# Kernel tuning notes

Hardware: AMD Instinct MI355X
Metric: run time of the kernel (lower is better)

The kernel has to match this reference:

```python
import jax, jax.numpy as jnp
import numpy as np

B, C, H, W = 2, 96, 40, 40
DIN, N, R, K = 192, 16, 6, 4  # d_inner, d_state, dt_rank, k_group


def silu(x):
    return x * jax.nn.sigmoid(x)


def dwconv3x3(x, w, b):
    # depthwise 3x3, SAME padding; w: (DIN,1,3,3)
    y = jax.lax.conv_general_dilated(x, w, (1, 1), [(1, 1), (1, 1)],
                                     feature_group_count=x.shape[1])
    return y + b[None, :, None, None]


def cross_scan(x):
    # (B,C,H,W) -> (B,4,C,L): row-major, col-major, and their reverses
    b, c, h, w = x.shape
    x0 = x.reshape(b, c, h * w)
    x1 = x.transpose(0, 1, 3, 2).reshape(b, c, h * w)
    return jnp.stack([x0, x1, x0[..., ::-1], x1[..., ::-1]], axis=1)


def cross_merge(y, h, w):
    # (B,4,C,H,W) -> (B,C,L)
    b, k, c = y.shape[0], y.shape[1], y.shape[2]
    y = y.reshape(b, k, c, h * w)
    y = y[:, :2] + y[:, 2:][..., ::-1]
    y1 = y[:, 1].reshape(b, c, w, h).transpose(0, 1, 3, 2).reshape(b, c, h * w)
    return y[:, 0] + y1


def selective_scan(u, dt, A, Bm, Cm, Dv, dbias):
    # u, dt: (B,K,DIN,L); A: (K*DIN,N); Bm, Cm: (B,K,N,L); Dv: (K*DIN,); dbias: (K*DIN,)
    b, k, d, l = u.shape
    n = A.shape[1]
    A4 = A.reshape(k, d, n)
    dt = jax.nn.softplus(dt + dbias.reshape(1, k, d, 1))
    # discretize: dA = exp(dt*A), dBu = dt*B*u  -> shapes (B,K,D,L,N)
    dA = jnp.exp(dt[..., None] * A4[None, :, :, None, :])
    dBu = dt[..., None] * Bm.transpose(0, 1, 3, 2)[:, :, None, :, :] * u[..., None]

    def combine(c1, c2):
        a1, b1 = c1
        a2, b2 = c2
        return a1 * a2, a2 * b1 + b2

    _, h = jax.lax.associative_scan(combine, (dA, dBu), axis=3)  # h: (B,K,D,L,N)
    y = jnp.einsum('bkdln,bknl->bkdl', h, Cm)
    return y + Dv.reshape(1, k, d, 1) * u


def ln2d(x, g, b):
    # LayerNorm over channel dim (channel_first LayerNorm2d)
    mu = x.mean(axis=1, keepdims=True)
    var = jnp.mean((x - mu) ** 2, axis=1, keepdims=True)
    xn = (x - mu) / jnp.sqrt(var + 1e-5)
    return xn * g[None, :, None, None] + b[None, :, None, None]


def setup_inputs():
    key = jax.random.key(0)
    ks = jax.random.split(key, 24)

    def rn(k, shape, s=0.02):
        return jax.random.normal(k, shape, dtype=jnp.float32) * s

    A_log = jnp.tile(jnp.log(jnp.arange(1, N + 1, dtype=jnp.float32))[None, :], (K * DIN, 1))
    return {
        'x_rgb': jax.random.normal(ks[0], (B, C, H, W), jnp.float32),
        'x_e': jax.random.normal(ks[1], (B, C, H, W), jnp.float32),
        'in_proj_w': rn(ks[2], (DIN, C)),
        'in_proj_mx_w': rn(ks[3], (DIN, C)),
        'conv_w': rn(ks[4], (DIN, 1, 3, 3), 0.1),
        'conv_b': jnp.zeros((DIN,), jnp.float32),
        'xproj1_w': rn(ks[5], (K, R + 2 * N, DIN)),
        'xproj2_w': rn(ks[6], (K, R + 2 * N, DIN)),
        'dtproj1_w': rn(ks[7], (K, DIN, R), 0.1),
        'dtproj1_b': rn(ks[8], (K, DIN), 0.1) - 4.0,
        'dtproj2_w': rn(ks[9], (K, DIN, R), 0.1),
        'dtproj2_b': rn(ks[10], (K, DIN), 0.1) - 4.0,
        'A_log_1': A_log,
        'A_log_2': A_log,
        'D_1': jnp.ones((K * DIN,), jnp.float32),
        'D_2': jnp.ones((K * DIN,), jnp.float32),
        'norm1_g': jnp.ones((DIN,), jnp.float32),
        'norm1_b': jnp.zeros((DIN,), jnp.float32),
        'norm2_g': jnp.ones((DIN,), jnp.float32),
        'norm2_b': jnp.zeros((DIN,), jnp.float32),
        'fc1_w1': rn(ks[11], (DIN // 16, DIN), 0.05),
        'fc1_w2': rn(ks[12], (DIN, DIN // 16), 0.05),
        'fc2_w1': rn(ks[13], (DIN // 16, DIN), 0.05),
        'fc2_w2': rn(ks[14], (DIN, DIN // 16), 0.05),
        'out_proj_w': rn(ks[15], (C, 2 * DIN)),
    }


def reference(x_rgb, x_e, in_proj_w, in_proj_mx_w, conv_w, conv_b, xproj1_w, xproj2_w,
              dtproj1_w, dtproj1_b, dtproj2_w, dtproj2_b, A_log_1, A_log_2, D_1, D_2,
              norm1_g, norm1_b, norm2_g, norm2_b, fc1_w1, fc1_w2, fc2_w1, fc2_w2, out_proj_w):
    # in_proj (1x1 conv style Linear2d)
    xr = jnp.einsum('oc,bchw->bohw', in_proj_w, x_rgb)
    xe = jnp.einsum('oc,bchw->bohw', in_proj_mx_w, x_e)
    # shared depthwise conv + SiLU
    xr = silu(dwconv3x3(xr, conv_w, conv_b))
    xe = silu(dwconv3x3(xe, conv_w, conv_b))
    b, d, h, w = xr.shape

    xs_r = cross_scan(xr)  # (B,K,DIN,L)
    xs_e = cross_scan(xe)

    def proj(xs, xp_w, dt_w):
        t = jnp.einsum('bkdl,kcd->bkcl', xs, xp_w)  # grouped 1x1 conv1d
        dts, Bm, Cm = jnp.split(t, [R, R + N], axis=2)
        dts = jnp.einsum('bkrl,kdr->bkdl', dts, dt_w)
        return dts, Bm, Cm

    d_r, B_r, C_r = proj(xs_r, xproj1_w, dtproj1_w)
    d_e, B_e, C_e = proj(xs_e, xproj2_w, dtproj2_w)

    # cross attention: rgb scan consumes C and D of the other modality
    y_r = selective_scan(xs_r, d_r, -jnp.exp(A_log_1), B_r, C_e, D_2, dtproj1_b.reshape(-1))
    y_e = selective_scan(xs_e, d_e, -jnp.exp(A_log_2), B_e, C_r, D_1, dtproj2_b.reshape(-1))

    y_r = cross_merge(y_r.reshape(b, K, d, h, w), h, w).reshape(b, d, h, w)
    y_e = cross_merge(y_e.reshape(b, K, d, h, w), h, w).reshape(b, d, h, w)
    y_r = ln2d(y_r, norm1_g, norm1_b)
    y_e = ln2d(y_e, norm2_g, norm2_b)

    # cross squeeze-excitation
    sq_r = xr.mean(axis=(2, 3))
    sq_e = xe.mean(axis=(2, 3))
    exc_r = jax.nn.sigmoid(silu(sq_r @ fc1_w1.T) @ fc1_w2.T)
    exc_e = jax.nn.sigmoid(silu(sq_e @ fc2_w1.T) @ fc2_w2.T)
    y_r = y_r * exc_e[:, :, None, None]
    y_e = y_e * exc_r[:, :, None, None]

    y = jnp.concatenate([y_r, y_e], axis=1)  # (B, 2*DIN, H, W)
    return jnp.einsum('oc,bchw->bohw', out_proj_w, y)
```

## Files before the change

kernel.cpp:

```cpp
#include <hip/hip_runtime.h>
#include <math.h>

#define BN   2
#define CIN  96
#define HH   40
#define WW   40
#define LL   1600
#define DIN  192
#define NS   16
#define RR   6
#define KK   4
#define CH   25

__device__ __forceinline__ float sigmoidf_(float x){ return 1.0f/(1.0f+expf(-x)); }
__device__ __forceinline__ float softplus_fast(float x){
  return x > 20.0f ? x : __logf(1.0f + __expf(x));
}

__device__ __forceinline__ void pow_tree(float R, float* p){
  float R2 = R * R;
  float R4 = R2 * R2;
  float R8 = R4 * R4;
  p[0]  = R;        p[1]  = R2;       p[2]  = R2 * R;   p[3]  = R4;
  p[4]  = R4 * R;   p[5]  = R4 * R2;  p[6]  = R4 * p[2];p[7]  = R8;
  p[8]  = R8 * R;   p[9]  = R8 * R2;  p[10] = R8 * p[2];p[11] = R8 * R4;
  p[12] = R8 * p[4];p[13] = R8 * p[5];p[14] = R8 * p[6];p[15] = R8 * R8;
}

__global__ void k_inproj(const float* __restrict__ x_rgb, const float* __restrict__ x_e,
                         const float* __restrict__ w_rgb, const float* __restrict__ w_e,
                         float* __restrict__ xproj){
  __shared__ float xin[16][100];
  int l0 = blockIdx.x * 16;
  int mb = blockIdx.y;
  int m = mb / BN, b = mb % BN;
  const float* xsrc = (m == 0 ? x_rgb : x_e) + (size_t)b * CIN * LL;
  const float* w    = (m == 0 ? w_rgb : w_e);
  for (int idx = threadIdx.x; idx < CIN * 16; idx += 256){
    int c = idx >> 4, px = idx & 15;
    xin[px][c] = xsrc[c * LL + l0 + px];
  }
  __syncthreads();
  int px = threadIdx.x & 15;
  int o0 = (threadIdx.x >> 4) * 12;
  float acc[12];
  #pragma unroll
  for (int i = 0; i < 12; ++i) acc[i] = 0.f;
  const float4* xv = reinterpret_cast<const float4*>(xin[px]);
  for (int cc = 0; cc < CIN / 4; ++cc){
    float4 x4 = xv[cc];
    #pragma unroll
    for (int i = 0; i < 12; ++i){
      float4 w4 = *reinterpret_cast<const float4*>(w + (o0 + i) * CIN + cc * 4);
      acc[i] += w4.x * x4.x + w4.y * x4.y + w4.z * x4.z + w4.w * x4.w;
    }
  }
  #pragma unroll
  for (int i = 0; i < 12; ++i)
    xproj[((size_t)mb * DIN + o0 + i) * LL + l0 + px] = acc[i];
}

__global__ void k_conv(const float* __restrict__ xproj, const float* __restrict__ conv_w,
                       const float* __restrict__ conv_b, float* __restrict__ x_act,
                       float* __restrict__ x_actT, float* __restrict__ u_chA,
                       float* __restrict__ u_chT, float* __restrict__ sq){
  __shared__ float pl[LL];
  __shared__ float sact[LL + HH];
  __shared__ float red[4];
  int d  = blockIdx.x;
  int mb = blockIdx.y;
  const float* src = xproj + ((size_t)mb * DIN + d) * LL;
  for (int p = threadIdx.x; p < LL; p += blockDim.x) pl[p] = src[p];
  __syncthreads();
  float cw[9];
  #pragma unroll
  for (int j = 0; j < 9; ++j) cw[j] = conv_w[d * 9 + j];
  float bias = conv_b[d];
  float* dst = x_act + ((size_t)mb * DIN + d) * LL;
  float lsum = 0.f;
  for (int p = threadIdx.x; p < LL; p += blockDim.x){
    int py = p / WW, px = p % WW;
    float acc = bias;
    #pragma unroll
    for (int dy = -1; dy <= 1; ++dy){
      int yy = py + dy;
      if (yy < 0 || yy >= HH) continue;
      #pragma unroll
      for (int dx = -1; dx <= 1; ++dx){
        int xx = px + dx;
        if (xx < 0 || xx >= WW) continue;
        acc += cw[(dy + 1) * 3 + (dx + 1)] * pl[yy * WW + xx];
      }
    }
    float s = acc * sigmoidf_(acc);
    dst[p] = s;
    sact[p + p / WW] = s;
    lsum += s;
  }
  #pragma unroll
  for (int off = 32; off; off >>= 1) lsum += __shfl_down(lsum, off);
  if ((threadIdx.x & 63) == 0) red[threadIdx.x >> 6] = lsum;
  __syncthreads();
  if (threadIdx.x == 0)
    sq[mb * DIN + d] = (red[0] + red[1] + red[2] + red[3]) * (1.0f / LL);
  size_t po = ((size_t)mb * DIN + d) * LL;
  float* dstT = x_actT + po;
  float* uA   = u_chA + po;
  float* uT   = u_chT + po;
  for (int q = threadIdx.x; q < LL; q += blockDim.x){
    int lt = (q % WW) * WW + q / WW;
    dstT[q] = sact[lt + lt / WW];
    int l = (q & 63) * CH + (q >> 6);
    uA[q] = sact[l + l / WW];
    int pt = (l % WW) * WW + l / WW;
    uT[q] = sact[pt + pt / WW];
  }
}

__global__ void k_xproj(const float* __restrict__ x_act, const float* __restrict__ x_actT,
                        const float* __restrict__ xp1, const float* __restrict__ xp2,
                        float* __restrict__ tdt_ch, float* __restrict__ B_ch,
                        float* __restrict__ C_ch){
  int l0 = blockIdx.x * 64;
  int k  = blockIdx.y;
  int mb = blockIdx.z; int m = mb / BN;
  const float* xw = (m == 0 ? xp1 : xp2) + k * 38 * DIN;
  const float* xa = ((k & 1) ? x_actT : x_act) + (size_t)mb * DIN * LL;
  bool rev = (k >= 2);
  int ll = threadIdx.x & 63;
  int g  = threadIdx.x >> 6;
  int c0 = g * 10;
  int l  = l0 + ll; if (rev) l = LL - 1 - l;
  const float* xcol = xa + l;
  float acc[10];
  #pragma unroll
  for (int i = 0; i < 10; ++i) acc[i] = 0.f;
  if (g < 3){
    for (int dd = 0; dd < DIN; ++dd){
      float xv = xcol[(size_t)dd * LL];
      #pragma unroll
      for (int i = 0; i < 10; ++i) acc[i] += xw[(c0 + i) * DIN + dd] * xv;
    }
  } else {
    for (int dd = 0; dd < DIN; ++dd){
      float xv = xcol[(size_t)dd * LL];
      #pragma unroll
      for (int i = 0; i < 8; ++i) acc[i] += xw[(c0 + i) * DIN + dd] * xv;
    }
  }
  int mbk = mb * KK + k;
  int lq = l0 + ll;
  int q = (lq % CH) * 64 + lq / CH;
  int nc = (g < 3) ? 10 : 8;
  for (int i = 0; i < nc; ++i){
    int c = c0 + i;
    float v = acc[i];
    if (c < RR){
      tdt_ch[((size_t)mbk * RR + c) * LL + q] = v;
    } else if (c < RR + NS){
      int n = c - RR;
      B_ch[(((size_t)mbk * 4 + (n >> 2)) * LL + q) * 4 + (n & 3)] = v;
    } else {
      int n = c - RR - NS;
      C_ch[(((size_t)mbk * 4 + (n >> 2)) * LL + q) * 4 + (n & 3)] = v;
    }
  }
}

__global__ void __launch_bounds__(256, 3) k_scan(
    const float* __restrict__ u_chA, const float* __restrict__ u_chT,
    const float* __restrict__ tdt_all, const float* __restrict__ B_ch,
    const float* __restrict__ C_ch,
    const float* __restrict__ Alog1, const float* __restrict__ Alog2,
    const float* __restrict__ D1, const float* __restrict__ D2,
    const float* __restrict__ dtw1, const float* __restrict__ dtb1,
    const float* __restrict__ dtw2, const float* __restrict__ dtb2,
    float* __restrict__ y_px){
  __shared__ float ystage[4][LL];
  __shared__ float dt_lds[4][LL];
  int wv   = threadIdx.x >> 6;
  int lane = threadIdx.x & 63;
  int chain = blockIdx.x * 4 + wv;
  int d   = chain % DIN;
  int mbk = chain / DIN;
  int k   = mbk % KK;
  int mb  = mbk / KK;
  int m = mb / BN, b = mb % BN;
  int kd = k * DIN + d;
  bool rev = (k >= 2);

  const float* Alog = (m == 0 ? Alog1 : Alog2) + kd * NS;
  float An[NS];
  bool fastA = true;
  #pragma unroll
  for (int n = 0; n < NS; ++n){
    An[n] = -__expf(Alog[n]);
    fastA = fastA && (fabsf(An[n] + (float)(n + 1)) <= 1e-4f * (float)(n + 1));
  }
  float Dv = (m == 0 ? D2 : D1)[kd];
  const float* dtw = (m == 0 ? dtw1 : dtw2) + kd * RR;
  float w0 = dtw[0], w1 = dtw[1], w2 = dtw[2], w3 = dtw[3], w4 = dtw[4], w5 = dtw[5];
  float dbias = (m == 0 ? dtb1 : dtb2)[kd];

  const float* t0 = tdt_all + (size_t)mbk * RR * LL;
  for (int s = 0; s < CH; ++s){
    int q = s * 64 + lane;
    float dtpre = w0 * t0[q] + w1 * t0[LL + q] + w2 * t0[2 * LL + q]
                + w3 * t0[3 * LL + q] + w4 * t0[4 * LL + q] + w5 * t0[5 * LL + q] + dbias;
    dt_lds[wv][q] = softplus_fast(dtpre);
  }

  const float4* B0 = reinterpret_cast<const float4*>(B_ch) + (size_t)mbk * 4 * LL;
  int mbk_o = ((1 - m) * BN + b) * KK + k;
  const float4* C0 = reinterpret_cast<const float4*>(C_ch) + (size_t)mbk_o * 4 * LL;
  const float* urow = ((k & 1) ? u_chT : u_chA) + ((size_t)mb * DIN + d) * LL;

  float h[NS];
  #pragma unroll
  for (int n = 0; n < NS; ++n) h[n] = 0.f;
  float Sdt = 0.f;

  if (fastA){
    #pragma unroll 5
    for (int s = 0; s < CH; ++s){
      int q = s * 64 + lane;
      float dt = dt_lds[wv][q];
      Sdt += dt;
      float u  = urow[rev ? (LL - 1 - q) : q];
      float du = dt * u;
      float4 b0 = B0[q], b1 = B0[LL + q], b2 = B0[2 * LL + q], b3 = B0[3 * LL + q];
      float4 c0 = C0[q], c1 = C0[LL + q], c2 = C0[2 * LL + q], c3 = C0[3 * LL + q];
      float Bv[NS] = {b0.x,b0.y,b0.z,b0.w, b1.x,b1.y,b1.z,b1.w,
                      b2.x,b2.y,b2.z,b2.w, b3.x,b3.y,b3.z,b3.w};
      float Cv[NS] = {c0.x,c0.y,c0.z,c0.w, c1.x,c1.y,c1.z,c1.w,
                      c2.x,c2.y,c2.z,c2.w, c3.x,c3.y,c3.z,c3.w};
      float p[NS];
      pow_tree(__expf(-dt), p);
      float y0 = Dv * u, y1 = 0.f, y2 = 0.f, y3 = 0.f;
      #pragma unroll
      for (int n = 0; n < NS; ++n){
        h[n] = p[n] * h[n] + du * Bv[n];
        float t = h[n] * Cv[n];
        if      ((n & 3) == 0) y0 += t;
        else if ((n & 3) == 1) y1 += t;
        else if ((n & 3) == 2) y2 += t;
        else                   y3 += t;
      }
      ystage[wv][lane * CH + s] = (y0 + y1) + (y2 + y3);
    }
  } else {
    #pragma unroll 5
    for (int s = 0; s < CH; ++s){
      int q = s * 64 + lane;
      float dt = dt_lds[wv][q];
      Sdt += dt;
      float u  = urow[rev ? (LL - 1 - q) : q];
      float du = dt * u;
      float4 b0 = B0[q], b1 = B0[LL + q], b2 = B0[2 * LL + q], b3 = B0[3 * LL + q];
      float4 c0 = C0[q], c1 = C0[LL + q], c2 = C0[2 * LL + q], c3 = C0[3 * LL + q];
      float Bv[NS] = {b0.x,b0.y,b0.z,b0.w, b1.x,b1.y,b1.z,b1.w,
                      b2.x,b2.y,b2.z,b2.w, b3.x,b3.y,b3.z,b3.w};
      float Cv[NS] = {c0.x,c0.y,c0.z,c0.w, c1.x,c1.y,c1.z,c1.w,
                      c2.x,c2.y,c2.z,c2.w, c3.x,c3.y,c3.z,c3.w};
      float y0 = Dv * u, y1 = 0.f, y2 = 0.f, y3 = 0.f;
      #pragma unroll
      for (int n = 0; n < NS; ++n){
        float dA = __expf(dt * An[n]);
        h[n] = dA * h[n] + du * Bv[n];
        float t = h[n] * Cv[n];
        if      ((n & 3) == 0) y0 += t;
        else if ((n & 3) == 1) y1 += t;
        else if ((n & 3) == 2) y2 += t;
        else                   y3 += t;
      }
      ystage[wv][lane * CH + s] = (y0 + y1) + (y2 + y3);
    }
  }
  float aP[NS];
  if (fastA){
    pow_tree(__expf(-Sdt), aP);
  } else {
    #pragma unroll
    for (int n = 0; n < NS; ++n) aP[n] = __expf(Sdt * An[n]);
  }

  #pragma unroll
  for (int off = 1; off < 64; off <<= 1){
    #pragma unroll
    for (int n = 0; n < NS; ++n){
      float ap = __shfl_up(aP[n], off);
      float bp = __shfl_up(h[n],  off);
      if (lane >= off){
        h[n]  = aP[n] * bp + h[n];
        aP[n] = aP[n] * ap;
      }
    }
  }
  #pragma unroll
  for (int n = 0; n < NS; ++n){
    float v = __shfl_up(h[n], 1);
    h[n] = (lane == 0) ? 0.f : v;
  }

  if (fastA){
    float cum = 0.f;
    #pragma unroll 5
    for (int s = 0; s < CH; ++s){
      int q = s * 64 + lane;
      cum += dt_lds[wv][q];
      float Rc = __expf(-cum);
      float4 c0 = C0[q], c1 = C0[LL + q], c2 = C0[2 * LL + q], c3 = C0[3 * LL + q];
      float Cv[NS] = {c0.x,c0.y,c0.z,c0.w, c1.x,c1.y,c1.z,c1.w,
                      c2.x,c2.y,c2.z,c2.w, c3.x,c3.y,c3.z,c3.w};
      float p[NS];
      pow_tree(Rc, p);
      float s0 = 0.f, s1 = 0.f, s2 = 0.f, s3 = 0.f;
      #pragma unroll
      for (int n = 0; n < NS; ++n){
        float t = h[n] * p[n] * Cv[n];
        if      ((n & 3) == 0) s0 += t;
        else if ((n & 3) == 1) s1 += t;
        else if ((n & 3) == 2) s2 += t;
        else                   s3 += t;
      }
      ystage[wv][lane * CH + s] += (s0 + s1) + (s2 + s3);
    }
  } else {
    float cum = 0.f;
    #pragma unroll 5
    for (int s = 0; s < CH; ++s){
      int q = s * 64 + lane;
      cum += dt_lds[wv][q];
      float4 c0 = C0[q], c1 = C0[LL + q], c2 = C0[2 * LL + q], c3 = C0[3 * LL + q];
      float Cv[NS] = {c0.x,c0.y,c0.z,c0.w, c1.x,c1.y,c1.z,c1.w,
                      c2.x,c2.y,c2.z,c2.w, c3.x,c3.y,c3.z,c3.w};
      float s0 = 0.f, s1 = 0.f, s2 = 0.f, s3 = 0.f;
      #pragma unroll
      for (int n = 0; n < NS; ++n){
        float t = h[n] * __expf(cum * An[n]) * Cv[n];
        if      ((n & 3) == 0) s0 += t;
        else if ((n & 3) == 1) s1 += t;
        else if ((n & 3) == 2) s2 += t;
        else                   s3 += t;
      }
      ystage[wv][lane * CH + s] += (s0 + s1) + (s2 + s3);
    }
  }

  float* yo = y_px + (size_t)chain * LL;
  for (int qq = lane; qq < LL; qq += 64){
    int l;
    if      (k == 0) l = qq;
    else if (k == 1) l = (qq % WW) * WW + qq / WW;
    else if (k == 2) l = LL - 1 - qq;
    else             { int qt = (qq % WW) * WW + qq / WW; l = LL - 1 - qt; }
    yo[qq] = ystage[wv][l];
  }
}

__global__ void __launch_bounds__(256) k_mergeout(
    const float* __restrict__ y_px, const float* __restrict__ sq,
    const float* __restrict__ fc1_w1, const float* __restrict__ fc1_w2,
    const float* __restrict__ fc2_w1, const float* __restrict__ fc2_w2,
    const float* __restrict__ n1g, const float* __restrict__ n1b,
    const float* __restrict__ n2g, const float* __restrict__ n2b,
    const float* __restrict__ wout, float* __restrict__ out){
  __shared__ float acc[2 * DIN][9];
  __shared__ float yt[8][388];
  __shared__ float ps[2][8][16], ps2[2][8][16];
  __shared__ float mu_s[2][8], inv_s[2][8];
  __shared__ float sqs[2][DIN];
  __shared__ float hid[2][12];
  __shared__ float exc_s[2][DIN];
  int p0 = blockIdx.x * 8;
  int b  = blockIdx.y;
  int tid = threadIdx.x;
  for (int idx = tid; idx < 2 * DIN * 8; idx += 256){
    int pp = idx & 7, row = idx >> 3;
    int mm = (row >= DIN), dd = row - mm * DIN;
    const float* yb = y_px + ((size_t)(mm * BN + b) * KK * DIN + dd) * LL + p0 + pp;
    acc[row][pp] = yb[0] + yb[(size_t)DIN * LL]
                 + yb[2 * (size_t)DIN * LL] + yb[3 * (size_t)DIN * LL];
  }
  for (int i = tid; i < 2 * DIN; i += 256){
    int mm = (i >= DIN), dd = i - mm * DIN;
    sqs[mm][dd] = sq[((1 - mm) * BN + b) * DIN + dd];
  }
  __syncthreads();
  if (tid < 24){
    int mm = tid / 12, j = tid - mm * 12;
    const float* w1 = (mm == 1 ? fc1_w1 : fc2_w1);
    float a = 0.f;
    for (int cch = 0; cch < DIN; ++cch) a += w1[j * DIN + cch] * sqs[mm][cch];
    hid[mm][j] = a * sigmoidf_(a);
  }
  {
    int pp = tid & 7, mm = (tid >> 3) & 1, g = tid >> 4;
    float s = 0.f, s2 = 0.f;
    #pragma unroll 4
    for (int j = 0; j < 12; ++j){
      float v = acc[mm * DIN + g * 12 + j][pp];
      s += v; s2 += v * v;
    }
    ps[mm][pp][g] = s; ps2[mm][pp][g] = s2;
  }
  __syncthreads();
  if (tid < 16){
    int mm = tid >> 3, pp = tid & 7;
    float s = 0.f, s2 = 0.f;
    #pragma unroll
    for (int g = 0; g < 16; ++g){ s += ps[mm][pp][g]; s2 += ps2[mm][pp][g]; }
    float mu  = s * (1.0f / DIN);
    float var = s2 * (1.0f / DIN) - mu * mu;
    mu_s[mm][pp] = mu; inv_s[mm][pp] = rsqrtf(var + 1e-5f);
  }
  for (int i = tid; i < 2 * DIN; i += 256){
    int mm = (i >= DIN), dd = i - mm * DIN;
    const float* w2 = (mm == 1 ? fc1_w2 : fc2_w2);
    float e = 0.f;
    #pragma unroll
    for (int j = 0; j < 12; ++j) e += w2[dd * 12 + j] * hid[mm][j];
    exc_s[mm][dd] = sigmoidf_(e);
  }
  __syncthreads();
  for (int idx = tid; idx < 2 * DIN * 8; idx += 256){
    int pp = idx & 7, row = idx >> 3;
    int mm = (row >= DIN), dd = row - mm * DIN;
    float g  = (mm ? n2g : n1g)[dd];
    float bb = (mm ? n2b : n1b)[dd];
    float v = (acc[row][pp] - mu_s[mm][pp]) * inv_s[mm][pp] * g + bb;
    yt[pp][row] = v * exc_s[mm][dd];
  }
  __syncthreads();
  int pp = tid & 7;
  int o0 = (tid >> 3) * 3;
  float a3[3] = {0.f, 0.f, 0.f};
  const float4* yv = reinterpret_cast<const float4*>(yt[pp]);
  for (int cc = 0; cc < 96; ++cc){
    float4 x4 = yv[cc];
    #pragma unroll
    for (int i = 0; i < 3; ++i){
      float4 w4 = *reinterpret_cast<const float4*>(wout + (o0 + i) * 2 * DIN + cc * 4);
      a3[i] += w4.x * x4.x + w4.y * x4.y + w4.z * x4.z + w4.w * x4.w;
    }
  }
  #pragma unroll
  for (int i = 0; i < 3; ++i)
    out[((size_t)b * CIN + o0 + i) * LL + p0 + pp] = a3[i];
}

extern "C" void kernel_launch(void* const* d_in, const int* in_sizes, int n_in,
                              void* d_out, int out_size, void* d_ws, size_t ws_size,
                              hipStream_t stream){
  const float* x_rgb   = (const float*)d_in[0];
  const float* x_e     = (const float*)d_in[1];
  const float* in_w    = (const float*)d_in[2];
  const float* in_mx_w = (const float*)d_in[3];
  const float* conv_w  = (const float*)d_in[4];
  const float* conv_b  = (const float*)d_in[5];
  const float* xp1     = (const float*)d_in[6];
  const float* xp2     = (const float*)d_in[7];
  const float* dtw1    = (const float*)d_in[8];
  const float* dtb1    = (const float*)d_in[9];
  const float* dtw2    = (const float*)d_in[10];
  const float* dtb2    = (const float*)d_in[11];
  const float* Alog1   = (const float*)d_in[12];
  const float* Alog2   = (const float*)d_in[13];
  const float* D1      = (const float*)d_in[14];
  const float* D2      = (const float*)d_in[15];
  const float* n1g     = (const float*)d_in[16];
  const float* n1b     = (const float*)d_in[17];
  const float* n2g     = (const float*)d_in[18];
  const float* n2b     = (const float*)d_in[19];
  const float* fc1_w1  = (const float*)d_in[20];
  const float* fc1_w2  = (const float*)d_in[21];
  const float* fc2_w1  = (const float*)d_in[22];
  const float* fc2_w2  = (const float*)d_in[23];
  const float* wout    = (const float*)d_in[24];

  float* ws = (float*)d_ws;
  float* u_chA   = ws;
  float* u_chT   = ws + 1228800;
  float* x_act   = ws + 2457600;
  float* x_actT  = ws + 3686400;
  float* xproj   = ws + 4915200;
  float* y_px    = ws + 6144000;
  float* B_ch    = ws + 11059200;
  float* C_ch    = ws + 11468800;
  float* tdt_ch  = ws + 11878400;
  float* sq      = ws + 12032000;

  k_inproj  <<<dim3(LL / 16, 2 * BN), 256, 0, stream>>>(x_rgb, x_e, in_w, in_mx_w, xproj);
  k_conv    <<<dim3(DIN, 2 * BN), 256, 0, stream>>>(xproj, conv_w, conv_b,
                                                    x_act, x_actT, u_chA, u_chT, sq);
  k_xproj   <<<dim3(LL / 64, KK, 2 * BN), 256, 0, stream>>>(x_act, x_actT, xp1, xp2,
                                                            tdt_ch, B_ch, C_ch);
  k_scan    <<<768, 256, 0, stream>>>(u_chA, u_chT, tdt_ch, B_ch, C_ch,
                                      Alog1, Alog2, D1, D2,
                                      dtw1, dtb1, dtw2, dtb2, y_px);
  k_mergeout<<<dim3(LL / 8, BN), 256, 0, stream>>>(y_px, sq,
                                                   fc1_w1, fc1_w2, fc2_w1, fc2_w2,
                                                   n1g, n1b, n2g, n2b,
                                                   wout, (float*)d_out);
}
```

Baseline: 174.0 us.

## Stage scan outputs in fp16 LDS, prefetch next chunk, raise occupancy

The per-wave staging buffer for scan outputs in the scan kernel changes from fp32 to fp16, halving its LDS footprint. Launch bounds rise from 3 to 4 blocks per SM to use the freed LDS. In the fast-A path, the B, C, u and dt loads for the next step are software-prefetched into registers so they overlap the current step's recurrence. The prefetch adds register pressure against the tighter launch bound, which may cause spills. fp16 staging also loses precision in the intermediate y values, and the second pass rounds to fp16 twice.

```diff
diff --git a/kernel.cpp b/kernel.cpp
--- a/kernel.cpp
+++ b/kernel.cpp
@@ -167,7 +167,7 @@
   }
 }
 
-__global__ void __launch_bounds__(256, 3) k_scan(
+__global__ void __launch_bounds__(256, 4) k_scan(
     const float* __restrict__ u_chA, const float* __restrict__ u_chT,
     const float* __restrict__ tdt_all, const float* __restrict__ B_ch,
     const float* __restrict__ C_ch,
@@ -176,7 +176,7 @@
     const float* __restrict__ dtw1, const float* __restrict__ dtb1,
     const float* __restrict__ dtw2, const float* __restrict__ dtb2,
     float* __restrict__ y_px){
-  __shared__ float ystage[4][LL];
+  __shared__ _Float16 ysth[4][LL];
   __shared__ float dt_lds[4][LL];
   int wv   = threadIdx.x >> 6;
   int lane = threadIdx.x & 63;
@@ -221,15 +221,28 @@
   float Sdt = 0.f;
 
   if (fastA){
+    float4 bP[4], cP[4]; float uP, dtP;
+    {
+      int q0 = lane;
+      dtP = dt_lds[wv][q0];
+      uP  = urow[rev ? (LL - 1 - q0) : q0];
+      bP[0]=B0[q0]; bP[1]=B0[LL+q0]; bP[2]=B0[2*LL+q0]; bP[3]=B0[3*LL+q0];
+      cP[0]=C0[q0]; cP[1]=C0[LL+q0]; cP[2]=C0[2*LL+q0]; cP[3]=C0[3*LL+q0];
+    }
     #pragma unroll 5
     for (int s = 0; s < CH; ++s){
-      int q = s * 64 + lane;
-      float dt = dt_lds[wv][q];
+      float dt = dtP, u = uP;
+      float4 b0=bP[0], b1=bP[1], b2=bP[2], b3=bP[3];
+      float4 c0=cP[0], c1=cP[1], c2=cP[2], c3=cP[3];
+      if (s + 1 < CH){
+        int q1 = (s + 1) * 64 + lane;
+        dtP = dt_lds[wv][q1];
+        uP  = urow[rev ? (LL - 1 - q1) : q1];
+        bP[0]=B0[q1]; bP[1]=B0[LL+q1]; bP[2]=B0[2*LL+q1]; bP[3]=B0[3*LL+q1];
+        cP[0]=C0[q1]; cP[1]=C0[LL+q1]; cP[2]=C0[2*LL+q1]; cP[3]=C0[3*LL+q1];
+      }
       Sdt += dt;
-      float u  = urow[rev ? (LL - 1 - q) : q];
       float du = dt * u;
-      float4 b0 = B0[q], b1 = B0[LL + q], b2 = B0[2 * LL + q], b3 = B0[3 * LL + q];
-      float4 c0 = C0[q], c1 = C0[LL + q], c2 = C0[2 * LL + q], c3 = C0[3 * LL + q];
       float Bv[NS] = {b0.x,b0.y,b0.z,b0.w, b1.x,b1.y,b1.z,b1.w,
                       b2.x,b2.y,b2.z,b2.w, b3.x,b3.y,b3.z,b3.w};
       float Cv[NS] = {c0.x,c0.y,c0.z,c0.w, c1.x,c1.y,c1.z,c1.w,
@@ -246,7 +259,7 @@
         else if ((n & 3) == 2) y2 += t;
         else                   y3 += t;
       }
-      ystage[wv][lane * CH + s] = (y0 + y1) + (y2 + y3);
+      ysth[wv][lane * CH + s] = (_Float16)((y0 + y1) + (y2 + y3));
     }
   } else {
     #pragma unroll 5
@@ -273,7 +286,7 @@
         else if ((n & 3) == 2) y2 += t;
         else                   y3 += t;
       }
-      ystage[wv][lane * CH + s] = (y0 + y1) + (y2 + y3);
+      ysth[wv][lane * CH + s] = (_Float16)((y0 + y1) + (y2 + y3));
     }
   }
   float aP[NS];
@@ -303,13 +316,24 @@
   }
 
   if (fastA){
+    float4 cP[4]; float dtP;
+    {
+      int q0 = lane;
+      dtP = dt_lds[wv][q0];
+      cP[0]=C0[q0]; cP[1]=C0[LL+q0]; cP[2]=C0[2*LL+q0]; cP[3]=C0[3*LL+q0];
+    }
     float cum = 0.f;
     #pragma unroll 5
     for (int s = 0; s < CH; ++s){
-      int q = s * 64 + lane;
-      cum += dt_lds[wv][q];
+      float dt = dtP;
+      float4 c0=cP[0], c1=cP[1], c2=cP[2], c3=cP[3];
+      if (s + 1 < CH){
+        int q1 = (s + 1) * 64 + lane;
+        dtP = dt_lds[wv][q1];
+        cP[0]=C0[q1]; cP[1]=C0[LL+q1]; cP[2]=C0[2*LL+q1]; cP[3]=C0[3*LL+q1];
+      }
+      cum += dt;
       float Rc = __expf(-cum);
-      float4 c0 = C0[q], c1 = C0[LL + q], c2 = C0[2 * LL + q], c3 = C0[3 * LL + q];
       float Cv[NS] = {c0.x,c0.y,c0.z,c0.w, c1.x,c1.y,c1.z,c1.w,
                       c2.x,c2.y,c2.z,c2.w, c3.x,c3.y,c3.z,c3.w};
       float p[NS];
@@ -323,7 +347,8 @@
         else if ((n & 3) == 2) s2 += t;
         else                   s3 += t;
       }
-      ystage[wv][lane * CH + s] += (s0 + s1) + (s2 + s3);
+      int li = lane * CH + s;
+      ysth[wv][li] = (_Float16)((float)ysth[wv][li] + (s0 + s1) + (s2 + s3));
     }
   } else {
     float cum = 0.f;
@@ -343,7 +368,8 @@
         else if ((n & 3) == 2) s2 += t;
         else                   s3 += t;
       }
-      ystage[wv][lane * CH + s] += (s0 + s1) + (s2 + s3);
+      int li = lane * CH + s;
+      ysth[wv][li] = (_Float16)((float)ysth[wv][li] + (s0 + s1) + (s2 + s3));
     }
   }
 
@@ -354,7 +380,7 @@
     else if (k == 1) l = (qq % WW) * WW + qq / WW;
     else if (k == 2) l = LL - 1 - qq;
     else             { int qt = (qq % WW) * WW + qq / WW; l = LL - 1 - qt; }
-    yo[qq] = ystage[wv][l];
+    yo[qq] = (float)ysth[wv][l];
   }
 }
 
```

Measured after the change: 168.0 us. -3.4%, faster.
